# Kernel optimization log

Measured on AMD Instinct MI355X. Metric: run time of the kernel, lower is better.

## Reference

```python
import jax, jax.numpy as jnp
import numpy as np

N_NODES = 50000
N_EDGES = 1000000
HIDDEN = 64
NUM_GRAPHS = 512
EPS = 1e-5


def _instance_norm(x, seg, num_graphs):
    # per-graph, per-channel normalization (PyG InstanceNorm, affine=False)
    ones = jnp.ones((x.shape[0], 1), x.dtype)
    cnt = jnp.clip(jax.ops.segment_sum(ones, seg, num_segments=num_graphs), 1.0)
    mean = jax.ops.segment_sum(x, seg, num_segments=num_graphs) / cnt
    xc = x - mean[seg]
    var = jax.ops.segment_sum(xc * xc, seg, num_segments=num_graphs) / cnt
    return xc * jax.lax.rsqrt(var + EPS)[seg]


def setup_inputs() -> dict:
    key = jax.random.key(0)
    ks = jax.random.split(key, 10)
    emb = jax.random.normal(ks[0], (N_NODES, HIDDEN), jnp.float32)
    edge_index = jax.random.randint(ks[1], (2, N_EDGES), 0, N_NODES, jnp.int64 if jax.config.read('jax_enable_x64') else jnp.int32)
    batch = jnp.sort(jax.random.randint(ks[2], (N_NODES,), 0, NUM_GRAPHS))
    h = HIDDEN
    # channels = [2h, 4h, h, 1]
    W1 = jax.random.normal(ks[3], (2 * h, 4 * h), jnp.float32) * 0.05
    b1 = jnp.zeros((4 * h,), jnp.float32)
    W2 = jax.random.normal(ks[4], (4 * h, h), jnp.float32) * 0.05
    b2 = jnp.zeros((h,), jnp.float32)
    W3 = jax.random.normal(ks[5], (h, 1), jnp.float32) * 0.05
    b3 = jnp.zeros((1,), jnp.float32)
    return {"emb": emb, "W1": W1, "b1": b1, "W2": W2, "b2": b2,
            "W3": W3, "b3": b3, "edge_index": edge_index, "batch": batch}


def reference(emb, W1, b1, W2, b2, W3, b3, edge_index, batch):
    col, row = edge_index[0], edge_index[1]
    f12 = jnp.concatenate([emb[col], emb[row]], axis=-1)  # [E, 2h]
    seg = batch[col]  # per-edge graph id
    x = f12 @ W1 + b1                                      # [E, 4h]
    x = jax.nn.relu(_instance_norm(x, seg, NUM_GRAPHS))
    x = x @ W2 + b2                                        # [E, h]
    x = jax.nn.relu(_instance_norm(x, seg, NUM_GRAPHS))
    return x @ W3 + b3                                     # [E, 1]
```

## Files before the change

kernel.cpp:

```cpp
#include <hip/hip_runtime.h>
#include <hip/hip_bf16.h>
#include <hip/hip_fp8.h>

#define EDGES 1000000
#define NNODES 50000
#define NG 512
#define NTILES 15625
#define NCOLB 50176

typedef __attribute__((ext_vector_type(8))) short bf16x8;
typedef __attribute__((ext_vector_type(4))) float f32x4;
typedef __attribute__((ext_vector_type(2))) float f32x2;

__device__ __forceinline__ unsigned short f2bf(float f){
  unsigned u = __float_as_uint(f);
  u += 0x7fffu + ((u >> 16) & 1u);
  return (unsigned short)(u >> 16);
}
__device__ __forceinline__ float bf2f(unsigned short h){
  return __uint_as_float(((unsigned)h) << 16);
}
__device__ __forceinline__ unsigned pk2bf(float x, float y){
  __hip_bfloat162 h = __float22bfloat162_rn(make_float2(x, y));
  union { __hip_bfloat162 h; unsigned u; } cv; cv.h = h;
  return cv.u;
}

#if defined(__has_builtin)
#if __has_builtin(__builtin_amdgcn_cvt_pk_f32_fp8) && __has_builtin(__builtin_amdgcn_cvt_pk_fp8_f32)
#define HAS_HW_FP8 1
#endif
#endif

__device__ __forceinline__ void fp8x4_f32(unsigned u, float& x0, float& x1, float& x2, float& x3){
#ifdef HAS_HW_FP8
  f32x2 lo = __builtin_amdgcn_cvt_pk_f32_fp8((int)u, false);
  f32x2 hi = __builtin_amdgcn_cvt_pk_f32_fp8((int)u, true);
  x0 = lo[0]; x1 = lo[1]; x2 = hi[0]; x3 = hi[1];
#else
  __hip_fp8_e4m3 a, b, c, d;
  a.__x = u & 0xff; b.__x = (u >> 8) & 0xff; c.__x = (u >> 16) & 0xff; d.__x = (u >> 24) & 0xff;
  x0 = (float)a; x1 = (float)b; x2 = (float)c; x3 = (float)d;
#endif
}
__device__ __forceinline__ unsigned f32_fp8x4(float x0, float x1, float x2, float x3){
#ifdef HAS_HW_FP8
  int w = 0;
  w = __builtin_amdgcn_cvt_pk_fp8_f32(x0, x1, w, false);
  w = __builtin_amdgcn_cvt_pk_fp8_f32(x2, x3, w, true);
  return (unsigned)w;
#else
  __hip_fp8_e4m3 a(x0), b(x1), c(x2), d(x3);
  return (unsigned)a.__x | ((unsigned)b.__x << 8) | ((unsigned)c.__x << 16) | ((unsigned)d.__x << 24);
#endif
}

__device__ __forceinline__ int xcd_swizzle(int bid, int nb){
  int nb8 = nb & ~7;
  if (bid >= nb8) return bid;
  int per = nb8 >> 3;
  return (bid & 7) * per + (bid >> 3);
}

__global__ void prep_w(const float* __restrict__ W1, const float* __restrict__ W2,
                       unsigned short* __restrict__ w1tn, unsigned short* __restrict__ w2t){
  int j = blockIdx.x * 256 + threadIdx.x;
  if (j < 32768){
    int jj = j >> 6, k = j & 63;
    float v = (jj < 256) ? W1[k * 256 + jj] : W1[(k + 64) * 256 + (jj - 256)];
    w1tn[j] = f2bf(v);
  } else {
    int i = j - 32768;
    if (i < 16384){
      int n = i >> 8, k = i & 255;
      w2t[i] = f2bf(W2[k * 64 + n]);
    }
  }
}

__global__ void hists(const int* __restrict__ ei, const int* __restrict__ batch,
                      unsigned* __restrict__ hist, unsigned* __restrict__ chist){
  __shared__ unsigned h[NG];
  int t = threadIdx.x;
  h[t] = 0; h[t + 256] = 0;
  __syncthreads();
  for (int i = 0; i < 4; i++){
    int e = blockIdx.x * 1024 + i * 256 + t;
    if (e < EDGES){
      int cn = ei[e];
      atomicAdd(&chist[cn], 1u);
      atomicAdd(&h[batch[cn]], 1u);
    }
  }
  __syncthreads();
  atomicAdd(&hist[t], h[t]);
  atomicAdd(&hist[t + 256], h[t + 256]);
}

__global__ void col_scan1(const unsigned* __restrict__ chist, unsigned* __restrict__ cpre,
                          unsigned* __restrict__ bsum){
  __shared__ unsigned s[256];
  int t = threadIdx.x;
  int i = blockIdx.x * 256 + t;
  unsigned v = (i < NNODES) ? chist[i] : 0u;
  s[t] = v;
  __syncthreads();
  for (int o = 1; o < 256; o <<= 1){
    unsigned u = (t >= o) ? s[t - o] : 0u;
    __syncthreads();
    s[t] += u;
    __syncthreads();
  }
  cpre[i] = s[t] - v;
  if (t == 255) bsum[blockIdx.x] = s[255];
}

__global__ void col_scan2(unsigned* __restrict__ bsum){
  __shared__ unsigned s[256];
  int t = threadIdx.x;
  unsigned v = (t < 196) ? bsum[t] : 0u;
  s[t] = v;
  __syncthreads();
  for (int o = 1; o < 256; o <<= 1){
    unsigned u = (t >= o) ? s[t - o] : 0u;
    __syncthreads();
    s[t] += u;
    __syncthreads();
  }
  if (t < 196) bsum[t] = s[t] - v;
}

__global__ void col_scan3(unsigned* __restrict__ cpre, const unsigned* __restrict__ bsum){
  int i = blockIdx.x * 256 + threadIdx.x;
  cpre[i] += bsum[blockIdx.x];
}

__global__ void col_scatter(const int* __restrict__ ei, const int* __restrict__ batch,
                            unsigned* __restrict__ cpre, int4* __restrict__ emeta){
  for (int i = 0; i < 4; i++){
    int e = blockIdx.x * 1024 + i * 256 + threadIdx.x;
    if (e < EDGES){
      int cn = ei[e];
      int pos = (int)atomicAdd(&cpre[cn], 1u);
      emeta[pos] = make_int4(cn, ei[EDGES + e], batch[cn], e);
    }
  }
}

__global__ __launch_bounds__(256) void node_gemm(
    const float* __restrict__ emb, const unsigned short* __restrict__ w1tn,
    unsigned short* __restrict__ P)
{
  __shared__ unsigned short As[64 * 72];
  int t = threadIdx.x;
  int n0 = blockIdx.x * 64;
  {
    int nl = t >> 2, part = t & 3;
    int node = n0 + nl; if (node >= NNODES) node = 0;
    const float4* src = (const float4*)(emb + node * 64 + part * 16);
    float4 f0 = src[0], f1 = src[1], f2 = src[2], f3 = src[3];
    uint4* dst = (uint4*)(As + nl * 72 + part * 16);
    dst[0] = make_uint4(pk2bf(f0.x, f0.y), pk2bf(f0.z, f0.w), pk2bf(f1.x, f1.y), pk2bf(f1.z, f1.w));
    dst[1] = make_uint4(pk2bf(f2.x, f2.y), pk2bf(f2.z, f2.w), pk2bf(f3.x, f3.y), pk2bf(f3.z, f3.w));
  }
  __syncthreads();
  int w = t >> 6, lane = t & 63, q = lane >> 4, c = lane & 15;
  f32x4 acc[4][8];
  for (int a = 0; a < 4; a++) for (int b = 0; b < 8; b++) for (int r = 0; r < 4; r++) acc[a][b][r] = 0.f;
  for (int k0 = 0; k0 < 64; k0 += 32){
    bf16x8 af[4];
    for (int tt = 0; tt < 4; tt++) af[tt] = *(const bf16x8*)(As + (tt * 16 + c) * 72 + k0 + q * 8);
    for (int n4 = 0; n4 < 8; n4++){
      bf16x8 bw = *(const bf16x8*)(w1tn + (w * 128 + n4 * 16 + c) * 64 + k0 + q * 8);
      for (int tt = 0; tt < 4; tt++)
        acc[tt][n4] = __builtin_amdgcn_mfma_f32_16x16x32_bf16(af[tt], bw, acc[tt][n4], 0, 0, 0);
    }
  }
  for (int tt = 0; tt < 4; tt++){
    for (int r = 0; r < 4; r++){
      int node = n0 + tt * 16 + q * 4 + r;
      if (node < NNODES){
        unsigned short* dst = P + (size_t)node * 512 + w * 128 + c;
        for (int n4 = 0; n4 < 8; n4++) dst[n4 * 16] = f2bf(acc[tt][n4][r]);
      }
    }
  }
}

__global__ void conv_p8(const unsigned short* __restrict__ P, unsigned char* __restrict__ P8){
  int i4 = blockIdx.x * 256 + threadIdx.x;
  if (i4 >= (NNODES * 512) / 4) return;
  ushort4 v = *(const ushort4*)(P + (size_t)i4 * 4);
  unsigned pk = f32_fp8x4(bf2f(v.x), bf2f(v.y), bf2f(v.z), bf2f(v.w));
  *(unsigned*)(P8 + (size_t)i4 * 4) = pk;
}

__global__ __launch_bounds__(256) void k1_gather(
    const unsigned char* __restrict__ P8, const int4* __restrict__ emeta,
    float* __restrict__ sum1, float* __restrict__ sqs1)
{
  int lane = threadIdx.x & 63;
  int bid = xcd_swizzle(blockIdx.x, gridDim.x);
  int wid = (bid * 256 + threadIdx.x) >> 6;
  if (wid >= NTILES) return;
  int p0 = wid * 64;
  int4 me = emeta[p0 + lane];
  int c4 = lane * 4;
  int s0 = __builtin_amdgcn_readlane(me.z, 0);
  bool uni = (__ballot(me.z == s0) == ~0ull);
  float sm0 = 0.f, sm1 = 0.f, sm2 = 0.f, sm3 = 0.f;
  float q0 = 0.f, q1 = 0.f, q2 = 0.f, q3 = 0.f;
  if (uni){
    int cprev = __builtin_amdgcn_readlane(me.x, 0);
    float a0, a1, a2, a3;
    fp8x4_f32(*(const unsigned*)(P8 + (size_t)cprev * 512 + c4), a0, a1, a2, a3);
    unsigned cur[4];
    #pragma unroll
    for (int j = 0; j < 4; j++){
      int re = __builtin_amdgcn_readlane(me.y, j);
      cur[j] = *(const unsigned*)(P8 + (size_t)re * 512 + 256 + c4);
    }
    for (int eb = 0; eb < 64; eb += 4){
      unsigned nxt[4];
      if (eb < 60){
        #pragma unroll
        for (int j = 0; j < 4; j++){
          int re = __builtin_amdgcn_readlane(me.y, eb + 4 + j);
          nxt[j] = *(const unsigned*)(P8 + (size_t)re * 512 + 256 + c4);
        }
      }
      #pragma unroll
      for (int j = 0; j < 4; j++){
        int ce = __builtin_amdgcn_readlane(me.x, eb + j);
        if (ce != cprev){
          fp8x4_f32(*(const unsigned*)(P8 + (size_t)ce * 512 + c4), a0, a1, a2, a3);
          cprev = ce;
        }
        float b0, b1, b2, b3;
        fp8x4_f32(cur[j], b0, b1, b2, b3);
        float x0 = a0 + b0, x1 = a1 + b1, x2v = a2 + b2, x3 = a3 + b3;
        sm0 += x0; q0 += x0 * x0;
        sm1 += x1; q1 += x1 * x1;
        sm2 += x2v; q2 += x2v * x2v;
        sm3 += x3; q3 += x3 * x3;
      }
      #pragma unroll
      for (int j = 0; j < 4; j++) cur[j] = nxt[j];
    }
    float* sp = sum1 + s0 * 256 + c4;
    float* qp = sqs1 + s0 * 256 + c4;
    atomicAdd(sp + 0, sm0); atomicAdd(sp + 1, sm1); atomicAdd(sp + 2, sm2); atomicAdd(sp + 3, sm3);
    atomicAdd(qp + 0, q0);  atomicAdd(qp + 1, q1);  atomicAdd(qp + 2, q2);  atomicAdd(qp + 3, q3);
  } else {
    int cur = s0;
    int cprev = -1;
    float a0 = 0.f, a1 = 0.f, a2 = 0.f, a3 = 0.f;
    for (int e = 0; e < 64; e++){
      int ce = __builtin_amdgcn_readlane(me.x, e);
      int re = __builtin_amdgcn_readlane(me.y, e);
      if (ce != cprev){
        fp8x4_f32(*(const unsigned*)(P8 + (size_t)ce * 512 + c4), a0, a1, a2, a3);
        cprev = ce;
      }
      float b0, b1, b2, b3;
      fp8x4_f32(*(const unsigned*)(P8 + (size_t)re * 512 + 256 + c4), b0, b1, b2, b3);
      int s = __builtin_amdgcn_readlane(me.z, e);
      if (s != cur){
        float* sp = sum1 + cur * 256 + c4;
        float* qp = sqs1 + cur * 256 + c4;
        atomicAdd(sp + 0, sm0); atomicAdd(sp + 1, sm1); atomicAdd(sp + 2, sm2); atomicAdd(sp + 3, sm3);
        atomicAdd(qp + 0, q0);  atomicAdd(qp + 1, q1);  atomicAdd(qp + 2, q2);  atomicAdd(qp + 3, q3);
        sm0 = sm1 = sm2 = sm3 = 0.f; q0 = q1 = q2 = q3 = 0.f;
        cur = s;
      }
      float x0 = a0 + b0, x1 = a1 + b1, x2v = a2 + b2, x3 = a3 + b3;
      sm0 += x0; q0 += x0 * x0;
      sm1 += x1; q1 += x1 * x1;
      sm2 += x2v; q2 += x2v * x2v;
      sm3 += x3; q3 += x3 * x3;
    }
    float* sp = sum1 + cur * 256 + c4;
    float* qp = sqs1 + cur * 256 + c4;
    atomicAdd(sp + 0, sm0); atomicAdd(sp + 1, sm1); atomicAdd(sp + 2, sm2); atomicAdd(sp + 3, sm3);
    atomicAdd(qp + 0, q0);  atomicAdd(qp + 1, q1);  atomicAdd(qp + 2, q2);  atomicAdd(qp + 3, q3);
  }
}

__global__ void finalize1(const float* __restrict__ sum1, const float* __restrict__ sqs1,
                          const unsigned* __restrict__ hist, float* __restrict__ r1,
                          float* __restrict__ mr1){
  int i = blockIdx.x * 256 + threadIdx.x;
  int g = i >> 8;
  float cnt = fmaxf((float)hist[g], 1.f);
  float m = sum1[i] / cnt;
  float v = sqs1[i] / cnt - m * m;
  v = fmaxf(v, 0.f);
  float r = rsqrtf(v + 1e-5f);
  r1[i] = r;
  mr1[i] = m * r;
}

__global__ void finalize2(const float* __restrict__ sum2, const float* __restrict__ sqs2,
                          const unsigned* __restrict__ hist, float* __restrict__ r2,
                          float* __restrict__ mr2){
  int i = blockIdx.x * 256 + threadIdx.x;
  int g = i >> 6;
  float cnt = fmaxf((float)hist[g], 1.f);
  float m = sum2[i] / cnt;
  float v = sqs2[i] / cnt - m * m;
  v = fmaxf(v, 0.f);
  float r = rsqrtf(v + 1e-5f);
  r2[i] = r;
  mr2[i] = m * r;
}

__device__ __forceinline__ void k2_tail(
    const unsigned short* __restrict__ Y, const unsigned short* __restrict__ w2t,
    const int* __restrict__ segl, const short* __restrict__ rsegA,
    const unsigned char* __restrict__ rloA, int nrun,
    float* __restrict__ sum2, float* __restrict__ sqs2, unsigned short* __restrict__ x2t,
    int p0, int w, int q, int c)
{
  f32x4 acc2[4];
  for (int tt = 0; tt < 4; tt++) for (int r = 0; r < 4; r++) acc2[tt][r] = 0.f;
  int ch2 = w * 16 + c;
  for (int kc = 0; kc < 8; kc++){
    int k0 = kc * 32;
    bf16x8 bfr = *(const bf16x8*)(w2t + ch2 * 256 + k0 + q * 8);
    for (int tt = 0; tt < 4; tt++){
      bf16x8 afr = *(const bf16x8*)(Y + (tt * 16 + c) * 264 + k0 + q * 8);
      acc2[tt] = __builtin_amdgcn_mfma_f32_16x16x32_bf16(afr, bfr, acc2[tt], 0, 0, 0);
    }
  }
  if (nrun == 1){
    int s = segl[0];
    float sm = 0.f, sq = 0.f;
    for (int tt = 0; tt < 4; tt++)
      for (int r = 0; r < 4; r++){
        float v = acc2[tt][r];
        sm += v; sq += v * v;
      }
    sm += __shfl_xor(sm, 16); sq += __shfl_xor(sq, 16);
    sm += __shfl_xor(sm, 32); sq += __shfl_xor(sq, 32);
    if (q == 0){
      atomicAdd(&sum2[s * 64 + ch2], sm);
      atomicAdd(&sqs2[s * 64 + ch2], sq);
    }
  } else {
    for (int rr = 0; rr < nrun; rr++){
      int s = rsegA[rr], lo = rloA[rr], hi = rloA[rr + 1];
      float sm = 0.f, sq = 0.f;
      for (int tt = 0; tt < 4; tt++){
        int elb = tt * 16 + q * 4;
        for (int r = 0; r < 4; r++){
          int el = elb + r;
          if (el >= lo && el < hi){
            float v = acc2[tt][r];
            sm += v; sq += v * v;
          }
        }
      }
      sm += __shfl_xor(sm, 16); sq += __shfl_xor(sq, 16);
      sm += __shfl_xor(sm, 32); sq += __shfl_xor(sq, 32);
      if (q == 0){
        atomicAdd(&sum2[s * 64 + ch2], sm);
        atomicAdd(&sqs2[s * 64 + ch2], sq);
      }
    }
  }
  for (int tt = 0; tt < 4; tt++){
    uint2 pk;
    pk.x = pk2bf(acc2[tt][0], acc2[tt][1]);
    pk.y = pk2bf(acc2[tt][2], acc2[tt][3]);
    *(uint2*)(x2t + (size_t)ch2 * EDGES + p0 + tt * 16 + q * 4) = pk;
  }
}

__global__ __launch_bounds__(256) void k2_fused(
    const unsigned short* __restrict__ P, const unsigned short* __restrict__ w2t,
    const int4* __restrict__ emeta,
    const float* __restrict__ r1, const float* __restrict__ mr1,
    float* __restrict__ sum2, float* __restrict__ sqs2,
    unsigned short* __restrict__ x2t)
{
  __shared__ unsigned short Y[64 * 264];
  __shared__ int segl[64];
  __shared__ short rsegA[64];
  __shared__ unsigned char rloA[65];
  __shared__ int nrunS;
  int t = threadIdx.x;
  int bid = xcd_swizzle(blockIdx.x, gridDim.x);
  int p0 = bid * 64;
  int w = t >> 6, lane = t & 63, q = lane >> 4, c = lane & 15;
  int c4 = lane * 4;
  int elb0 = w * 16;
  int4 me = emeta[p0 + elb0 + (lane & 15)];

  ushort4 bb[16];
  #pragma unroll
  for (int e = 0; e < 16; e++){
    int re = __builtin_amdgcn_readlane(me.y, e);
    bb[e] = *(const ushort4*)(P + (size_t)re * 512 + 256 + c4);
  }
  int cprev = __builtin_amdgcn_readlane(me.x, 0);
  ushort4 a = *(const ushort4*)(P + (size_t)cprev * 512 + c4);
  int s0g = __builtin_amdgcn_readlane(me.z, 0);
  float4 r4  = *(const float4*)(r1  + s0g * 256 + c4);
  float4 mr4 = *(const float4*)(mr1 + s0g * 256 + c4);

  if (t < 64) segl[t] = emeta[p0 + t].z;
  if (w == 0){
    int sN = segl[lane];
    int nxt = (lane < 63) ? segl[lane + 1] : sN;
    unsigned long long mask = __ballot(sN != nxt);
    if (lane == 0){
      if (mask == 0ull){
        nrunS = 1; rloA[0] = 0; rloA[1] = 64; rsegA[0] = (short)sN;
      } else {
        int n = 0, cur = segl[0];
        rsegA[0] = (short)cur; rloA[0] = 0;
        for (int i = 1; i < 64; i++)
          if (segl[i] != cur){ cur = segl[i]; n++; rsegA[n] = (short)cur; rloA[n] = (unsigned char)i; }
        rloA[n + 1] = 64; nrunS = n + 1;
      }
    }
  }
  __syncthreads();
  int nrun = nrunS;
  bool uni = (nrun == 1);

  #pragma unroll
  for (int e = 0; e < 16; e++){
    int ce = __builtin_amdgcn_readlane(me.x, e);
    if (ce != cprev){ a = *(const ushort4*)(P + (size_t)ce * 512 + c4); cprev = ce; }
    float4 rr4 = r4, mm4 = mr4;
    if (!uni){
      int s = __builtin_amdgcn_readlane(me.z, e);
      rr4 = *(const float4*)(r1  + s * 256 + c4);
      mm4 = *(const float4*)(mr1 + s * 256 + c4);
    }
    float y0 = fmaxf(0.f, (bf2f(a.x) + bf2f(bb[e].x)) * rr4.x - mm4.x);
    float y1 = fmaxf(0.f, (bf2f(a.y) + bf2f(bb[e].y)) * rr4.y - mm4.y);
    float y2 = fmaxf(0.f, (bf2f(a.z) + bf2f(bb[e].z)) * rr4.z - mm4.z);
    float y3 = fmaxf(0.f, (bf2f(a.w) + bf2f(bb[e].w)) * rr4.w - mm4.w);
    uint2 pk;
    pk.x = pk2bf(y0, y1);
    pk.y = pk2bf(y2, y3);
    *(uint2*)(Y + (elb0 + e) * 264 + c4) = pk;
  }
  __syncthreads();
  k2_tail(Y, w2t, segl, rsegA, rloA, nrun, sum2, sqs2, x2t, p0, w, q, c);
}

__global__ __launch_bounds__(256) void k3_out(
    const unsigned short* __restrict__ x2t, const int4* __restrict__ emeta,
    const float* __restrict__ r2, const float* __restrict__ mr2,
    const float* __restrict__ W3, const float* __restrict__ b3, float* __restrict__ out)
{
  int pp4 = (blockIdx.x * 256 + threadIdx.x) * 4;
  if (pp4 >= EDGES) return;
  int4 m0 = emeta[pp4 + 0];
  int4 m1 = emeta[pp4 + 1];
  int4 m2 = emeta[pp4 + 2];
  int4 m3 = emeta[pp4 + 3];
  float a0 = 0.f, a1 = 0.f, a2 = 0.f, a3 = 0.f;
  if (m0.z == m3.z && m0.z == m1.z && m0.z == m2.z){
    const float* rp = r2  + m0.z * 64;
    const float* mp = mr2 + m0.z * 64;
    #pragma unroll 8
    for (int ch = 0; ch < 64; ch++){
      ushort4 v = *(const ushort4*)(x2t + (size_t)ch * EDGES + pp4);
      float rr = rp[ch], mm = mp[ch], wv = W3[ch];
      a0 += fmaxf(0.f, bf2f(v.x) * rr - mm) * wv;
      a1 += fmaxf(0.f, bf2f(v.y) * rr - mm) * wv;
      a2 += fmaxf(0.f, bf2f(v.z) * rr - mm) * wv;
      a3 += fmaxf(0.f, bf2f(v.w) * rr - mm) * wv;
    }
  } else {
    #pragma unroll 8
    for (int ch = 0; ch < 64; ch++){
      ushort4 v = *(const ushort4*)(x2t + (size_t)ch * EDGES + pp4);
      float wv = W3[ch];
      a0 += fmaxf(0.f, bf2f(v.x) * r2[m0.z * 64 + ch] - mr2[m0.z * 64 + ch]) * wv;
      a1 += fmaxf(0.f, bf2f(v.y) * r2[m1.z * 64 + ch] - mr2[m1.z * 64 + ch]) * wv;
      a2 += fmaxf(0.f, bf2f(v.z) * r2[m2.z * 64 + ch] - mr2[m2.z * 64 + ch]) * wv;
      a3 += fmaxf(0.f, bf2f(v.w) * r2[m3.z * 64 + ch] - mr2[m3.z * 64 + ch]) * wv;
    }
  }
  float bv = b3[0];
  out[m0.w] = a0 + bv;
  out[m1.w] = a1 + bv;
  out[m2.w] = a2 + bv;
  out[m3.w] = a3 + bv;
}

extern "C" void kernel_launch(void* const* d_in, const int* in_sizes, int n_in,
                              void* d_out, int out_size, void* d_ws, size_t ws_size,
                              hipStream_t stream)
{
  (void)in_sizes; (void)n_in; (void)out_size;
  const float* emb = (const float*)d_in[0];
  const float* W1  = (const float*)d_in[1];
  const float* W2  = (const float*)d_in[3];
  const float* W3  = (const float*)d_in[5];
  const float* b3  = (const float*)d_in[6];
  const int* ei    = (const int*)d_in[7];
  const int* batch = (const int*)d_in[8];
  float* out = (float*)d_out;

  char* p = (char*)d_ws;
  size_t off = 0;
  auto take = [&](size_t n) -> char* {
    char* r = p + off;
    off += (n + 255) & ~(size_t)255;
    return r;
  };

  unsigned short* w1tn = (unsigned short*)take(32768 * 2);
  unsigned short* w2t  = (unsigned short*)take(16384 * 2);
  int4* emeta = (int4*)take((size_t)EDGES * 16);
  unsigned short* P   = (unsigned short*)take((size_t)NNODES * 512 * 2);
  unsigned char*  P8  = (unsigned char*)take((size_t)NNODES * 512);
  unsigned short* x2t = (unsigned short*)take((size_t)EDGES * 64 * 2);
  float* r1  = (float*)take(512 * 256 * 4);
  float* mr1 = (float*)take(512 * 256 * 4);
  float* r2  = (float*)take(512 * 64 * 4);
  float* mr2 = (float*)take(512 * 64 * 4);
  unsigned* cpre = (unsigned*)take(NCOLB * 4);
  unsigned* bsum = (unsigned*)take(256 * 4);
  char* zbase = p + off;
  unsigned* hist  = (unsigned*)take(NG * 4);
  unsigned* chist = (unsigned*)take(NCOLB * 4);
  float* sum1 = (float*)take(512 * 256 * 4);
  float* sqs1 = (float*)take(512 * 256 * 4);
  float* sum2 = (float*)take(512 * 64 * 4);
  float* sqs2 = (float*)take(512 * 64 * 4);
  size_t zsize = (size_t)((p + off) - zbase);

  if (ws_size < off) return;

  hipMemsetAsync(zbase, 0, zsize, stream);
  prep_w<<<192, 256, 0, stream>>>(W1, W2, w1tn, w2t);
  hists<<<977, 256, 0, stream>>>(ei, batch, hist, chist);
  col_scan1<<<196, 256, 0, stream>>>(chist, cpre, bsum);
  col_scan2<<<1, 256, 0, stream>>>(bsum);
  col_scan3<<<196, 256, 0, stream>>>(cpre, bsum);
  col_scatter<<<977, 256, 0, stream>>>(ei, batch, cpre, emeta);
  node_gemm<<<(NNODES + 63) / 64, 256, 0, stream>>>(emb, w1tn, P);
  conv_p8<<<(NNODES * 512 / 4 + 255) / 256, 256, 0, stream>>>(P, P8);
  k1_gather<<<(NTILES + 3) / 4, 256, 0, stream>>>(P8, emeta, sum1, sqs1);
  finalize1<<<512, 256, 0, stream>>>(sum1, sqs1, hist, r1, mr1);
  k2_fused<<<NTILES, 256, 0, stream>>>(P, w2t, emeta, r1, mr1, sum2, sqs2, x2t);
  finalize2<<<128, 256, 0, stream>>>(sum2, sqs2, hist, r2, mr2);
  k3_out<<<977, 256, 0, stream>>>(x2t, emeta, r2, mr2, W3, b3, out);
}
```

Measured before the change: 590.9 us.

## Fuse independent launches and split graphs into halves to overlap gather with edge GEMM

Node GEMM and histogram now share one launch, as do edge scatter and the fp8 conversion of P, which removes separate launches and lets independent work run side by side. Graph ids are split at 256 into two halves. The layer-1 statistics gather for the upper half runs in the same launch as the layer-2 fused edge GEMM for tiles that end in the lower half, with the layer-1 finalize also done per half. The aim is to hide the tail and launch gaps between stages. In exchange, the combined phase2 kernel carries k2's large shared-memory footprint into k1 blocks, and the extra launches contain many blocks that exit early.

```diff
diff --git a/kernel.cpp b/kernel.cpp
--- a/kernel.cpp
+++ b/kernel.cpp
@@ -7,6 +7,11 @@
 #define NG 512
 #define NTILES 15625
 #define NCOLB 50176
+#define GEMMB 782
+#define HISTB 977
+#define CONVB 12500
+#define K1B 3907
+#define GSPLIT 256
 
 typedef __attribute__((ext_vector_type(8))) short bf16x8;
 typedef __attribute__((ext_vector_type(4))) float f32x4;
@@ -78,14 +83,53 @@
   }
 }
 
-__global__ void hists(const int* __restrict__ ei, const int* __restrict__ batch,
-                      unsigned* __restrict__ hist, unsigned* __restrict__ chist){
+__device__ void node_gemm_body(int bid, const float* __restrict__ emb,
+                               const unsigned short* __restrict__ w1tn,
+                               unsigned short* __restrict__ P){
+  __shared__ unsigned short As[64 * 72];
+  int t = threadIdx.x;
+  int n0 = bid * 64;
+  {
+    int nl = t >> 2, part = t & 3;
+    int node = n0 + nl; if (node >= NNODES) node = 0;
+    const float4* src = (const float4*)(emb + node * 64 + part * 16);
+    float4 f0 = src[0], f1 = src[1], f2 = src[2], f3 = src[3];
+    uint4* dst = (uint4*)(As + nl * 72 + part * 16);
+    dst[0] = make_uint4(pk2bf(f0.x, f0.y), pk2bf(f0.z, f0.w), pk2bf(f1.x, f1.y), pk2bf(f1.z, f1.w));
+    dst[1] = make_uint4(pk2bf(f2.x, f2.y), pk2bf(f2.z, f2.w), pk2bf(f3.x, f3.y), pk2bf(f3.z, f3.w));
+  }
+  __syncthreads();
+  int w = t >> 6, lane = t & 63, q = lane >> 4, c = lane & 15;
+  f32x4 acc[4][8];
+  for (int a = 0; a < 4; a++) for (int b = 0; b < 8; b++) for (int r = 0; r < 4; r++) acc[a][b][r] = 0.f;
+  for (int k0 = 0; k0 < 64; k0 += 32){
+    bf16x8 af[4];
+    for (int tt = 0; tt < 4; tt++) af[tt] = *(const bf16x8*)(As + (tt * 16 + c) * 72 + k0 + q * 8);
+    for (int n4 = 0; n4 < 8; n4++){
+      bf16x8 bw = *(const bf16x8*)(w1tn + (w * 128 + n4 * 16 + c) * 64 + k0 + q * 8);
+      for (int tt = 0; tt < 4; tt++)
+        acc[tt][n4] = __builtin_amdgcn_mfma_f32_16x16x32_bf16(af[tt], bw, acc[tt][n4], 0, 0, 0);
+    }
+  }
+  for (int tt = 0; tt < 4; tt++){
+    for (int r = 0; r < 4; r++){
+      int node = n0 + tt * 16 + q * 4 + r;
+      if (node < NNODES){
+        unsigned short* dst = P + (size_t)node * 512 + w * 128 + c;
+        for (int n4 = 0; n4 < 8; n4++) dst[n4 * 16] = f2bf(acc[tt][n4][r]);
+      }
+    }
+  }
+}
+
+__device__ void hists_body(int bid, const int* __restrict__ ei, const int* __restrict__ batch,
+                           unsigned* __restrict__ hist, unsigned* __restrict__ chist){
   __shared__ unsigned h[NG];
   int t = threadIdx.x;
   h[t] = 0; h[t + 256] = 0;
   __syncthreads();
   for (int i = 0; i < 4; i++){
-    int e = blockIdx.x * 1024 + i * 256 + t;
+    int e = bid * 1024 + i * 256 + t;
     if (e < EDGES){
       int cn = ei[e];
       atomicAdd(&chist[cn], 1u);
@@ -95,6 +139,14 @@
   __syncthreads();
   atomicAdd(&hist[t], h[t]);
   atomicAdd(&hist[t + 256], h[t + 256]);
+}
+
+__global__ __launch_bounds__(256) void gemm_hists(
+    const float* __restrict__ emb, const unsigned short* __restrict__ w1tn,
+    unsigned short* __restrict__ P, const int* __restrict__ ei,
+    const int* __restrict__ batch, unsigned* __restrict__ hist, unsigned* __restrict__ chist){
+  if (blockIdx.x < GEMMB) node_gemm_body(blockIdx.x, emb, w1tn, P);
+  else hists_body(blockIdx.x - GEMMB, ei, batch, hist, chist);
 }
 
 __global__ void col_scan1(const unsigned* __restrict__ chist, unsigned* __restrict__ cpre,
@@ -135,75 +187,39 @@
   cpre[i] += bsum[blockIdx.x];
 }
 
-__global__ void col_scatter(const int* __restrict__ ei, const int* __restrict__ batch,
-                            unsigned* __restrict__ cpre, int4* __restrict__ emeta){
-  for (int i = 0; i < 4; i++){
-    int e = blockIdx.x * 1024 + i * 256 + threadIdx.x;
-    if (e < EDGES){
-      int cn = ei[e];
-      int pos = (int)atomicAdd(&cpre[cn], 1u);
-      emeta[pos] = make_int4(cn, ei[EDGES + e], batch[cn], e);
-    }
-  }
-}
-
-__global__ __launch_bounds__(256) void node_gemm(
-    const float* __restrict__ emb, const unsigned short* __restrict__ w1tn,
-    unsigned short* __restrict__ P)
+__global__ void scatter_conv(const int* __restrict__ ei, const int* __restrict__ batch,
+                             unsigned* __restrict__ cpre, int4* __restrict__ emeta,
+                             const unsigned short* __restrict__ P, unsigned char* __restrict__ P8){
+  if (blockIdx.x < HISTB){
+    for (int i = 0; i < 4; i++){
+      int e = blockIdx.x * 1024 + i * 256 + threadIdx.x;
+      if (e < EDGES){
+        int cn = ei[e];
+        int pos = (int)atomicAdd(&cpre[cn], 1u);
+        emeta[pos] = make_int4(cn, ei[EDGES + e], batch[cn], e);
+      }
+    }
+  } else {
+    int i8 = (blockIdx.x - HISTB) * 256 + threadIdx.x;
+    if (i8 < (NNODES * 512) / 8){
+      const ushort4* vp = (const ushort4*)P + (size_t)i8 * 2;
+      ushort4 v0 = vp[0], v1 = vp[1];
+      uint2 o;
+      o.x = f32_fp8x4(bf2f(v0.x), bf2f(v0.y), bf2f(v0.z), bf2f(v0.w));
+      o.y = f32_fp8x4(bf2f(v1.x), bf2f(v1.y), bf2f(v1.z), bf2f(v1.w));
+      *((uint2*)P8 + i8) = o;
+    }
+  }
+}
+
+__device__ void k1_body(int wid, const unsigned char* __restrict__ P8, const int4* __restrict__ emeta,
+                        float* __restrict__ sum1, float* __restrict__ sqs1, int wantB)
 {
-  __shared__ unsigned short As[64 * 72];
-  int t = threadIdx.x;
-  int n0 = blockIdx.x * 64;
-  {
-    int nl = t >> 2, part = t & 3;
-    int node = n0 + nl; if (node >= NNODES) node = 0;
-    const float4* src = (const float4*)(emb + node * 64 + part * 16);
-    float4 f0 = src[0], f1 = src[1], f2 = src[2], f3 = src[3];
-    uint4* dst = (uint4*)(As + nl * 72 + part * 16);
-    dst[0] = make_uint4(pk2bf(f0.x, f0.y), pk2bf(f0.z, f0.w), pk2bf(f1.x, f1.y), pk2bf(f1.z, f1.w));
-    dst[1] = make_uint4(pk2bf(f2.x, f2.y), pk2bf(f2.z, f2.w), pk2bf(f3.x, f3.y), pk2bf(f3.z, f3.w));
-  }
-  __syncthreads();
-  int w = t >> 6, lane = t & 63, q = lane >> 4, c = lane & 15;
-  f32x4 acc[4][8];
-  for (int a = 0; a < 4; a++) for (int b = 0; b < 8; b++) for (int r = 0; r < 4; r++) acc[a][b][r] = 0.f;
-  for (int k0 = 0; k0 < 64; k0 += 32){
-    bf16x8 af[4];
-    for (int tt = 0; tt < 4; tt++) af[tt] = *(const bf16x8*)(As + (tt * 16 + c) * 72 + k0 + q * 8);
-    for (int n4 = 0; n4 < 8; n4++){
-      bf16x8 bw = *(const bf16x8*)(w1tn + (w * 128 + n4 * 16 + c) * 64 + k0 + q * 8);
-      for (int tt = 0; tt < 4; tt++)
-        acc[tt][n4] = __builtin_amdgcn_mfma_f32_16x16x32_bf16(af[tt], bw, acc[tt][n4], 0, 0, 0);
-    }
-  }
-  for (int tt = 0; tt < 4; tt++){
-    for (int r = 0; r < 4; r++){
-      int node = n0 + tt * 16 + q * 4 + r;
-      if (node < NNODES){
-        unsigned short* dst = P + (size_t)node * 512 + w * 128 + c;
-        for (int n4 = 0; n4 < 8; n4++) dst[n4 * 16] = f2bf(acc[tt][n4][r]);
-      }
-    }
-  }
-}
-
-__global__ void conv_p8(const unsigned short* __restrict__ P, unsigned char* __restrict__ P8){
-  int i4 = blockIdx.x * 256 + threadIdx.x;
-  if (i4 >= (NNODES * 512) / 4) return;
-  ushort4 v = *(const ushort4*)(P + (size_t)i4 * 4);
-  unsigned pk = f32_fp8x4(bf2f(v.x), bf2f(v.y), bf2f(v.z), bf2f(v.w));
-  *(unsigned*)(P8 + (size_t)i4 * 4) = pk;
-}
-
-__global__ __launch_bounds__(256) void k1_gather(
-    const unsigned char* __restrict__ P8, const int4* __restrict__ emeta,
-    float* __restrict__ sum1, float* __restrict__ sqs1)
-{
-  int lane = threadIdx.x & 63;
-  int bid = xcd_swizzle(blockIdx.x, gridDim.x);
-  int wid = (bid * 256 + threadIdx.x) >> 6;
   if (wid >= NTILES) return;
   int p0 = wid * 64;
+  int segFirst = ((const int*)emeta)[4 * p0 + 2];
+  if ((segFirst >= GSPLIT) != (wantB != 0)) return;
+  int lane = threadIdx.x & 63;
   int4 me = emeta[p0 + lane];
   int c4 = lane * 4;
   int s0 = __builtin_amdgcn_readlane(me.z, 0);
@@ -257,11 +273,11 @@
     float a0 = 0.f, a1 = 0.f, a2 = 0.f, a3 = 0.f;
     for (int e = 0; e < 64; e++){
       int ce = __builtin_amdgcn_readlane(me.x, e);
-      int re = __builtin_amdgcn_readlane(me.y, e);
       if (ce != cprev){
         fp8x4_f32(*(const unsigned*)(P8 + (size_t)ce * 512 + c4), a0, a1, a2, a3);
         cprev = ce;
       }
+      int re = __builtin_amdgcn_readlane(me.y, e);
       float b0, b1, b2, b3;
       fp8x4_f32(*(const unsigned*)(P8 + (size_t)re * 512 + 256 + c4), b0, b1, b2, b3);
       int s = __builtin_amdgcn_readlane(me.z, e);
@@ -286,111 +302,22 @@
   }
 }
 
-__global__ void finalize1(const float* __restrict__ sum1, const float* __restrict__ sqs1,
-                          const unsigned* __restrict__ hist, float* __restrict__ r1,
-                          float* __restrict__ mr1){
-  int i = blockIdx.x * 256 + threadIdx.x;
-  int g = i >> 8;
-  float cnt = fmaxf((float)hist[g], 1.f);
-  float m = sum1[i] / cnt;
-  float v = sqs1[i] / cnt - m * m;
-  v = fmaxf(v, 0.f);
-  float r = rsqrtf(v + 1e-5f);
-  r1[i] = r;
-  mr1[i] = m * r;
-}
-
-__global__ void finalize2(const float* __restrict__ sum2, const float* __restrict__ sqs2,
-                          const unsigned* __restrict__ hist, float* __restrict__ r2,
-                          float* __restrict__ mr2){
-  int i = blockIdx.x * 256 + threadIdx.x;
-  int g = i >> 6;
-  float cnt = fmaxf((float)hist[g], 1.f);
-  float m = sum2[i] / cnt;
-  float v = sqs2[i] / cnt - m * m;
-  v = fmaxf(v, 0.f);
-  float r = rsqrtf(v + 1e-5f);
-  r2[i] = r;
-  mr2[i] = m * r;
-}
-
-__device__ __forceinline__ void k2_tail(
-    const unsigned short* __restrict__ Y, const unsigned short* __restrict__ w2t,
-    const int* __restrict__ segl, const short* __restrict__ rsegA,
-    const unsigned char* __restrict__ rloA, int nrun,
-    float* __restrict__ sum2, float* __restrict__ sqs2, unsigned short* __restrict__ x2t,
-    int p0, int w, int q, int c)
+__device__ void k2_body(int tile, const unsigned short* __restrict__ P,
+                        const unsigned short* __restrict__ w2t, const int4* __restrict__ emeta,
+                        const float* __restrict__ r1, const float* __restrict__ mr1,
+                        float* __restrict__ sum2, float* __restrict__ sqs2,
+                        unsigned short* __restrict__ x2t, int wantB)
 {
-  f32x4 acc2[4];
-  for (int tt = 0; tt < 4; tt++) for (int r = 0; r < 4; r++) acc2[tt][r] = 0.f;
-  int ch2 = w * 16 + c;
-  for (int kc = 0; kc < 8; kc++){
-    int k0 = kc * 32;
-    bf16x8 bfr = *(const bf16x8*)(w2t + ch2 * 256 + k0 + q * 8);
-    for (int tt = 0; tt < 4; tt++){
-      bf16x8 afr = *(const bf16x8*)(Y + (tt * 16 + c) * 264 + k0 + q * 8);
-      acc2[tt] = __builtin_amdgcn_mfma_f32_16x16x32_bf16(afr, bfr, acc2[tt], 0, 0, 0);
-    }
-  }
-  if (nrun == 1){
-    int s = segl[0];
-    float sm = 0.f, sq = 0.f;
-    for (int tt = 0; tt < 4; tt++)
-      for (int r = 0; r < 4; r++){
-        float v = acc2[tt][r];
-        sm += v; sq += v * v;
-      }
-    sm += __shfl_xor(sm, 16); sq += __shfl_xor(sq, 16);
-    sm += __shfl_xor(sm, 32); sq += __shfl_xor(sq, 32);
-    if (q == 0){
-      atomicAdd(&sum2[s * 64 + ch2], sm);
-      atomicAdd(&sqs2[s * 64 + ch2], sq);
-    }
-  } else {
-    for (int rr = 0; rr < nrun; rr++){
-      int s = rsegA[rr], lo = rloA[rr], hi = rloA[rr + 1];
-      float sm = 0.f, sq = 0.f;
-      for (int tt = 0; tt < 4; tt++){
-        int elb = tt * 16 + q * 4;
-        for (int r = 0; r < 4; r++){
-          int el = elb + r;
-          if (el >= lo && el < hi){
-            float v = acc2[tt][r];
-            sm += v; sq += v * v;
-          }
-        }
-      }
-      sm += __shfl_xor(sm, 16); sq += __shfl_xor(sq, 16);
-      sm += __shfl_xor(sm, 32); sq += __shfl_xor(sq, 32);
-      if (q == 0){
-        atomicAdd(&sum2[s * 64 + ch2], sm);
-        atomicAdd(&sqs2[s * 64 + ch2], sq);
-      }
-    }
-  }
-  for (int tt = 0; tt < 4; tt++){
-    uint2 pk;
-    pk.x = pk2bf(acc2[tt][0], acc2[tt][1]);
-    pk.y = pk2bf(acc2[tt][2], acc2[tt][3]);
-    *(uint2*)(x2t + (size_t)ch2 * EDGES + p0 + tt * 16 + q * 4) = pk;
-  }
-}
-
-__global__ __launch_bounds__(256) void k2_fused(
-    const unsigned short* __restrict__ P, const unsigned short* __restrict__ w2t,
-    const int4* __restrict__ emeta,
-    const float* __restrict__ r1, const float* __restrict__ mr1,
-    float* __restrict__ sum2, float* __restrict__ sqs2,
-    unsigned short* __restrict__ x2t)
-{
+  int p0 = tile * 64;
+  int segLast = ((const int*)emeta)[4 * (p0 + 63) + 2];
+  if ((segLast >= GSPLIT) != (wantB != 0)) return;
+
   __shared__ unsigned short Y[64 * 264];
   __shared__ int segl[64];
   __shared__ short rsegA[64];
   __shared__ unsigned char rloA[65];
   __shared__ int nrunS;
   int t = threadIdx.x;
-  int bid = xcd_swizzle(blockIdx.x, gridDim.x);
-  int p0 = bid * 64;
   int w = t >> 6, lane = t & 63, q = lane >> 4, c = lane & 15;
   int c4 = lane * 4;
   int elb0 = w * 16;
@@ -449,7 +376,124 @@
     *(uint2*)(Y + (elb0 + e) * 264 + c4) = pk;
   }
   __syncthreads();
-  k2_tail(Y, w2t, segl, rsegA, rloA, nrun, sum2, sqs2, x2t, p0, w, q, c);
+
+  f32x4 acc2[4];
+  for (int tt = 0; tt < 4; tt++) for (int r = 0; r < 4; r++) acc2[tt][r] = 0.f;
+  int ch2 = w * 16 + c;
+  for (int kc = 0; kc < 8; kc++){
+    int k0 = kc * 32;
+    bf16x8 bfr = *(const bf16x8*)(w2t + ch2 * 256 + k0 + q * 8);
+    for (int tt = 0; tt < 4; tt++){
+      bf16x8 afr = *(const bf16x8*)(Y + (tt * 16 + c) * 264 + k0 + q * 8);
+      acc2[tt] = __builtin_amdgcn_mfma_f32_16x16x32_bf16(afr, bfr, acc2[tt], 0, 0, 0);
+    }
+  }
+
+  if (uni){
+    int s = segl[0];
+    float sm = 0.f, sq = 0.f;
+    for (int tt = 0; tt < 4; tt++)
+      for (int r = 0; r < 4; r++){
+        float v = acc2[tt][r];
+        sm += v; sq += v * v;
+      }
+    sm += __shfl_xor(sm, 16); sq += __shfl_xor(sq, 16);
+    sm += __shfl_xor(sm, 32); sq += __shfl_xor(sq, 32);
+    if (q == 0){
+      atomicAdd(&sum2[s * 64 + ch2], sm);
+      atomicAdd(&sqs2[s * 64 + ch2], sq);
+    }
+  } else {
+    for (int rr = 0; rr < nrun; rr++){
+      int s = rsegA[rr], lo = rloA[rr], hi = rloA[rr + 1];
+      float sm = 0.f, sq = 0.f;
+      for (int tt = 0; tt < 4; tt++){
+        int elb = tt * 16 + q * 4;
+        for (int r = 0; r < 4; r++){
+          int el = elb + r;
+          if (el >= lo && el < hi){
+            float v = acc2[tt][r];
+            sm += v; sq += v * v;
+          }
+        }
+      }
+      sm += __shfl_xor(sm, 16); sq += __shfl_xor(sq, 16);
+      sm += __shfl_xor(sm, 32); sq += __shfl_xor(sq, 32);
+      if (q == 0){
+        atomicAdd(&sum2[s * 64 + ch2], sm);
+        atomicAdd(&sqs2[s * 64 + ch2], sq);
+      }
+    }
+  }
+  for (int tt = 0; tt < 4; tt++){
+    uint2 pk;
+    pk.x = pk2bf(acc2[tt][0], acc2[tt][1]);
+    pk.y = pk2bf(acc2[tt][2], acc2[tt][3]);
+    *(uint2*)(x2t + (size_t)ch2 * EDGES + p0 + tt * 16 + q * 4) = pk;
+  }
+}
+
+__global__ __launch_bounds__(256) void k1_phase(
+    const unsigned char* __restrict__ P8, const int4* __restrict__ emeta,
+    float* __restrict__ sum1, float* __restrict__ sqs1, int wantB){
+  int bid = xcd_swizzle(blockIdx.x, gridDim.x);
+  int wid = (bid * 256 + threadIdx.x) >> 6;
+  k1_body(wid, P8, emeta, sum1, sqs1, wantB);
+}
+
+__global__ __launch_bounds__(256) void k2_phase(
+    const unsigned short* __restrict__ P, const unsigned short* __restrict__ w2t,
+    const int4* __restrict__ emeta, const float* __restrict__ r1, const float* __restrict__ mr1,
+    float* __restrict__ sum2, float* __restrict__ sqs2, unsigned short* __restrict__ x2t, int wantB){
+  int tile = xcd_swizzle(blockIdx.x, gridDim.x);
+  k2_body(tile, P, w2t, emeta, r1, mr1, sum2, sqs2, x2t, wantB);
+}
+
+__global__ __launch_bounds__(256) void phase2(
+    const unsigned char* __restrict__ P8, const unsigned short* __restrict__ P,
+    const unsigned short* __restrict__ w2t, const int4* __restrict__ emeta,
+    const float* __restrict__ r1, const float* __restrict__ mr1,
+    float* __restrict__ sum1, float* __restrict__ sqs1,
+    float* __restrict__ sum2, float* __restrict__ sqs2, unsigned short* __restrict__ x2t){
+  int bid = blockIdx.x;
+  int d5 = bid / 5;
+  if (bid - d5 * 5 == 0){
+    int sb = xcd_swizzle(d5, K1B);
+    int wid = (sb * 256 + threadIdx.x) >> 6;
+    k1_body(wid, P8, emeta, sum1, sqs1, 1);
+  } else {
+    int id = bid - d5 - 1;
+    int tile = xcd_swizzle(id, NTILES);
+    k2_body(tile, P, w2t, emeta, r1, mr1, sum2, sqs2, x2t, 0);
+  }
+}
+
+__global__ void finalize1(const float* __restrict__ sum1, const float* __restrict__ sqs1,
+                          const unsigned* __restrict__ hist, float* __restrict__ r1,
+                          float* __restrict__ mr1, int g0){
+  int i = g0 * 256 + blockIdx.x * 256 + threadIdx.x;
+  int g = i >> 8;
+  float cnt = fmaxf((float)hist[g], 1.f);
+  float m = sum1[i] / cnt;
+  float v = sqs1[i] / cnt - m * m;
+  v = fmaxf(v, 0.f);
+  float r = rsqrtf(v + 1e-5f);
+  r1[i] = r;
+  mr1[i] = m * r;
+}
+
+__global__ void finalize2(const float* __restrict__ sum2, const float* __restrict__ sqs2,
+                          const unsigned* __restrict__ hist, float* __restrict__ r2,
+                          float* __restrict__ mr2){
+  int i = blockIdx.x * 256 + threadIdx.x;
+  int g = i >> 6;
+  float cnt = fmaxf((float)hist[g], 1.f);
+  float m = sum2[i] / cnt;
+  float v = sqs2[i] / cnt - m * m;
+  v = fmaxf(v, 0.f);
+  float r = rsqrtf(v + 1e-5f);
+  r2[i] = r;
+  mr2[i] = m * r;
 }
 
 __global__ __launch_bounds__(256) void k3_out(
@@ -541,16 +585,16 @@
 
   hipMemsetAsync(zbase, 0, zsize, stream);
   prep_w<<<192, 256, 0, stream>>>(W1, W2, w1tn, w2t);
-  hists<<<977, 256, 0, stream>>>(ei, batch, hist, chist);
+  gemm_hists<<<GEMMB + HISTB, 256, 0, stream>>>(emb, w1tn, P, ei, batch, hist, chist);
   col_scan1<<<196, 256, 0, stream>>>(chist, cpre, bsum);
   col_scan2<<<1, 256, 0, stream>>>(bsum);
   col_scan3<<<196, 256, 0, stream>>>(cpre, bsum);
-  col_scatter<<<977, 256, 0, stream>>>(ei, batch, cpre, emeta);
-  node_gemm<<<(NNODES + 63) / 64, 256, 0, stream>>>(emb, w1tn, P);
-  conv_p8<<<(NNODES * 512 / 4 + 255) / 256, 256, 0, stream>>>(P, P8);
-  k1_gather<<<(NTILES + 3) / 4, 256, 0, stream>>>(P8, emeta, sum1, sqs1);
-  finalize1<<<512, 256, 0, stream>>>(sum1, sqs1, hist, r1, mr1);
-  k2_fused<<<NTILES, 256, 0, stream>>>(P, w2t, emeta, r1, mr1, sum2, sqs2, x2t);
+  scatter_conv<<<HISTB + CONVB, 256, 0, stream>>>(ei, batch, cpre, emeta, P, P8);
+  k1_phase<<<K1B, 256, 0, stream>>>(P8, emeta, sum1, sqs1, 0);
+  finalize1<<<256, 256, 0, stream>>>(sum1, sqs1, hist, r1, mr1, 0);
+  phase2<<<K1B + NTILES, 256, 0, stream>>>(P8, P, w2t, emeta, r1, mr1, sum1, sqs1, sum2, sqs2, x2t);
+  finalize1<<<256, 256, 0, stream>>>(sum1, sqs1, hist, r1, mr1, GSPLIT);
+  k2_phase<<<NTILES, 256, 0, stream>>>(P, w2t, emeta, r1, mr1, sum2, sqs2, x2t, 1);
   finalize2<<<128, 256, 0, stream>>>(sum2, sqs2, hist, r2, mr2);
   k3_out<<<977, 256, 0, stream>>>(x2t, emeta, r2, mr2, W3, b3, out);
 }
```

Measured after the change: 776.4 us. 1.31x slower.
